# Kernel tuning notes

Measured on AMD Instinct MI355X. Metric: run time of the kernel, lower is better.

The kernel has to match this reference:

```python
import jax, jax.numpy as jnp
import numpy as np

N, DIM, K = 8192, 64, 32
ALPHA = 1.0

def setup_inputs() -> dict:
    key = jax.random.key(0)
    k1, k2, k3, k4, k5, k6 = jax.random.split(key, 6)
    s = 1.0 / np.sqrt(DIM)
    return {
        "node_emb": jax.random.normal(k1, (N, DIM), dtype=jnp.float32),
        "noise": jax.random.uniform(k2, (N, N), dtype=jnp.float32),
        "W1": jax.random.uniform(k3, (DIM, DIM), minval=-s, maxval=s, dtype=jnp.float32),
        "b1": jax.random.uniform(k4, (DIM,), minval=-s, maxval=s, dtype=jnp.float32),
        "W2": jax.random.uniform(k5, (DIM, DIM), minval=-s, maxval=s, dtype=jnp.float32),
        "b2": jax.random.uniform(k6, (DIM,), minval=-s, maxval=s, dtype=jnp.float32),
    }

def reference(node_emb, noise, W1, b1, W2, b2):
    # dual Linear + exact (erf) GELU, matching torch F.gelu default
    v1 = jax.nn.gelu(ALPHA * (node_emb @ W1.T + b1), approximate=False)  # [N, dim]
    v2 = jax.nn.gelu(ALPHA * (node_emb @ W2.T + b2), approximate=False)  # [N, dim]
    # asymmetric adjacency: relu(v1 v2^T - v2 v1^T)  -> [N, N]
    adj = jax.nn.relu(v1 @ v2.T - v2 @ v1.T)
    # top-k per row on noise-perturbed scores (tie-break), scatter 1s into mask
    _, idx = jax.lax.top_k(adj + noise * 0.01, K)            # idx: [N, K]
    mask = jnp.zeros((N, N), dtype=adj.dtype).at[jnp.arange(N)[:, None], idx].set(1.0)
    return adj * mask
```

## Files before the change

### kernel.cpp

```cpp
#include <hip/hip_runtime.h>
#include <math.h>


__global__ __launch_bounds__(256) void compute_vv(
    const float* __restrict__ emb, const float* __restrict__ W1,
    const float* __restrict__ b1, const float* __restrict__ W2,
    const float* __restrict__ b2, float* __restrict__ VV)
{
    __shared__ float sW[2][64 * 65];
    __shared__ float sb[2][64];
    __shared__ float semb[2][64];
    int tid = threadIdx.x;
    for (int t = tid; t < 64 * 64; t += 256) {
        int o = t >> 6, k = t & 63;
        sW[0][o * 65 + k] = W1[t];
        sW[1][o * 65 + k] = W2[t];
    }
    if (tid < 64) { sb[0][tid] = b1[tid]; sb[1][tid] = b2[tid]; }
    int i0 = blockIdx.x * 2;
    if (tid < 128) semb[tid >> 6][tid & 63] = emb[(size_t)i0 * 64 + tid];
    __syncthreads();

    int li = tid >> 7;
    int c  = tid & 127;
    int o  = c >> 1;
    int w  = c & 1;
    const float* wr = &sW[w][o * 65];
    const float* e  = &semb[li][0];
    float acc = 0.0f;
#pragma unroll
    for (int k = 0; k < 64; ++k) acc = fmaf(e[k], wr[k], acc);
    float x = acc + sb[w][o];
    double xd = (double)x;
    double g = 0.5 * xd * (1.0 + erf(xd * 0.70710678118654752440));
    VV[(size_t)(i0 + li) * 128 + c] = (float)g;
}

__global__ __launch_bounds__(256, 3) void adj_gemm_tri(
    const float* __restrict__ VV, float* __restrict__ out)
{
    int bi = blockIdx.x, bj = blockIdx.y;
    if (bj < bi) return;

    __shared__ __align__(16) float smem[8448];
    float* Ar1 = smem;
    float* Ar2 = smem + 2112;
    float* Ac1 = smem + 4224;
    float* Ac2 = smem + 6336;

    int tid  = threadIdx.x;
    int trow = tid >> 4, tcol = tid & 15;
    const int grow = bi * 128, gcol = bj * 128;

    float d1[8][8], d2[8][8];
#pragma unroll
    for (int r = 0; r < 8; ++r)
#pragma unroll
        for (int c = 0; c < 8; ++c) { d1[r][c] = 0.0f; d2[r][c] = 0.0f; }

    const float4* VV4 = (const float4*)VV;
    for (int kb = 0; kb < 4; ++kb) {
        __syncthreads();
#pragma unroll
        for (int g4 = 0; g4 < 4; ++g4) {
            int g = tid + g4 * 256;
            int row = g >> 3, off = g & 7;
            float4 f = VV4[(size_t)(grow + row) * 32 + kb * 8 + off];
            float4 h = VV4[(size_t)(gcol + row) * 32 + kb * 8 + off];
            int kk = off * 2;
            Ar1[kk * 132 + row] = f.x; Ar2[kk * 132 + row] = f.y;
            Ar1[(kk + 1) * 132 + row] = f.z; Ar2[(kk + 1) * 132 + row] = f.w;
            Ac1[kk * 132 + row] = h.x; Ac2[kk * 132 + row] = h.y;
            Ac1[(kk + 1) * 132 + row] = h.z; Ac2[(kk + 1) * 132 + row] = h.w;
        }
        __syncthreads();
#pragma unroll 2
        for (int k = 0; k < 16; ++k) {
            float rv1[8], rv2[8], cv1[8], cv2[8];
            *(float4*)&rv1[0] = *(const float4*)&Ar1[k * 132 + trow * 4];
            *(float4*)&rv1[4] = *(const float4*)&Ar1[k * 132 + 64 + trow * 4];
            *(float4*)&rv2[0] = *(const float4*)&Ar2[k * 132 + trow * 4];
            *(float4*)&rv2[4] = *(const float4*)&Ar2[k * 132 + 64 + trow * 4];
            *(float4*)&cv1[0] = *(const float4*)&Ac1[k * 132 + tcol * 4];
            *(float4*)&cv1[4] = *(const float4*)&Ac1[k * 132 + 64 + tcol * 4];
            *(float4*)&cv2[0] = *(const float4*)&Ac2[k * 132 + tcol * 4];
            *(float4*)&cv2[4] = *(const float4*)&Ac2[k * 132 + 64 + tcol * 4];
#pragma unroll
            for (int r = 0; r < 8; ++r)
#pragma unroll
                for (int c = 0; c < 8; ++c) {
                    d1[r][c] = fmaf(rv1[r], cv2[c], d1[r][c]);
                    d2[r][c] = fmaf(rv2[r], cv1[c], d2[r][c]);
                }
        }
    }

#pragma unroll
    for (int rr = 0; rr < 8; ++rr) {
        int r = (rr < 4) ? (trow * 4 + rr) : (64 + trow * 4 + (rr - 4));
        float4 o0, o1;
        o0.x = fmaxf(d1[rr][0] - d2[rr][0], 0.0f);
        o0.y = fmaxf(d1[rr][1] - d2[rr][1], 0.0f);
        o0.z = fmaxf(d1[rr][2] - d2[rr][2], 0.0f);
        o0.w = fmaxf(d1[rr][3] - d2[rr][3], 0.0f);
        o1.x = fmaxf(d1[rr][4] - d2[rr][4], 0.0f);
        o1.y = fmaxf(d1[rr][5] - d2[rr][5], 0.0f);
        o1.z = fmaxf(d1[rr][6] - d2[rr][6], 0.0f);
        o1.w = fmaxf(d1[rr][7] - d2[rr][7], 0.0f);
        float* op = out + (size_t)(grow + r) * 8192 + gcol;
        *(float4*)(op + tcol * 4)      = o0;
        *(float4*)(op + 64 + tcol * 4) = o1;
    }

    float (*tT)[132] = (float(*)[132])smem;
#pragma unroll
    for (int p = 0; p < 2; ++p) {
        __syncthreads();
#pragma unroll
        for (int cc4 = 0; cc4 < 4; ++cc4) {
            int cc = p * 4 + cc4;
            int cl = tcol * 4 + cc4;
            float4 lo, hi;
            lo.x = fmaxf(d2[0][cc] - d1[0][cc], 0.0f);
            lo.y = fmaxf(d2[1][cc] - d1[1][cc], 0.0f);
            lo.z = fmaxf(d2[2][cc] - d1[2][cc], 0.0f);
            lo.w = fmaxf(d2[3][cc] - d1[3][cc], 0.0f);
            hi.x = fmaxf(d2[4][cc] - d1[4][cc], 0.0f);
            hi.y = fmaxf(d2[5][cc] - d1[5][cc], 0.0f);
            hi.z = fmaxf(d2[6][cc] - d1[6][cc], 0.0f);
            hi.w = fmaxf(d2[7][cc] - d1[7][cc], 0.0f);
            *(float4*)&tT[cl][trow * 4]      = lo;
            *(float4*)&tT[cl][64 + trow * 4] = hi;
        }
        __syncthreads();
        for (int g = tid; g < 2048; g += 256) {
            int orow_ = g >> 5, off = g & 31;
            float4 v = *(const float4*)&tT[orow_][off * 4];
            *(float4*)(out + (size_t)(gcol + p * 64 + orow_) * 8192 + grow + off * 4) = v;
        }
    }
}

#define SKIPV 0.015625f
#define CAP   1024

__device__ __forceinline__ int binof(float s, float lo, float scale, float inv) {
    int b = (int)((s - lo) * scale);
    if (b > 1023) b = 1023;
    if (lo + (float)b * inv > s) --b;
    else if (b < 1023 && lo + (float)(b + 1) * inv <= s) ++b;
    return b;
}

__device__ __forceinline__ void select_bin1024(
    const unsigned* __restrict__ hist, unsigned* __restrict__ chs,
    int tid, int krem, int* __restrict__ sh_bin, int* __restrict__ sh_above,
    unsigned* __restrict__ sh_total)
{
    chs[tid] = hist[tid * 4 + 0] + hist[tid * 4 + 1] +
               hist[tid * 4 + 2] + hist[tid * 4 + 3];
    __syncthreads();
    if (tid < 64) {
        unsigned g = chs[tid * 4 + 0] + chs[tid * 4 + 1] +
                     chs[tid * 4 + 2] + chs[tid * 4 + 3];
        unsigned v = g;
#pragma unroll
        for (int off = 1; off < 64; off <<= 1) {
            unsigned o = __shfl_down(v, off);
            if (tid + off < 64) v += o;
        }
        if (tid == 0) *sh_total = v;
        unsigned above = v - g;
        if (above < (unsigned)krem && (unsigned)krem <= above + g) {
            unsigned cum = above;
            int bin = -1;
            for (int c = 3; c >= 0 && bin < 0; --c) {
                unsigned cs = chs[tid * 4 + c];
                if (cum + cs >= (unsigned)krem) {
                    int cb = tid * 4 + c;
                    for (int b = 3; b >= 0; --b) {
                        unsigned h = hist[cb * 4 + b];
                        if (cum + h >= (unsigned)krem) { bin = cb * 4 + b; break; }
                        cum += h;
                    }
                } else cum += cs;
            }
            *sh_bin = bin; *sh_above = (int)cum;
        }
    }
    __syncthreads();
}

__global__ __launch_bounds__(256, 4) void topk_linear(
    const float* __restrict__ noise, float* __restrict__ out)
{
    __shared__ unsigned hist[1024];
    __shared__ unsigned chs[256];
    __shared__ float    cs[CAP];
    __shared__ int      ci[CAP];
    __shared__ unsigned flags[256];
    __shared__ int      sh_bin, sh_above;
    __shared__ unsigned sh_total, sh_cnt;

    int tid = threadIdx.x;
    int row = blockIdx.x;
    float*       orow = out   + (size_t)row * 8192;
    const float* nrow = noise + (size_t)row * 8192;
    const float4* o4 = (const float4*)orow;
    const float4* n4 = (const float4*)nrow;

    float4 nv[8], av[8];
#pragma unroll
    for (int i = 0; i < 8; ++i) nv[i] = n4[tid + i * 256];
#pragma unroll
    for (int i = 0; i < 8; ++i) av[i] = o4[tid + i * 256];

    for (int i = tid; i < 1024; i += 256) hist[i] = 0u;
    flags[tid] = 0u;

    float ss[32];
#pragma unroll
    for (int i = 0; i < 8; ++i) {
        ss[i * 4 + 0] = __fadd_rn(av[i].x, __fmul_rn(nv[i].x, 0.01f));
        ss[i * 4 + 1] = __fadd_rn(av[i].y, __fmul_rn(nv[i].y, 0.01f));
        ss[i * 4 + 2] = __fadd_rn(av[i].z, __fmul_rn(nv[i].z, 0.01f));
        ss[i * 4 + 3] = __fadd_rn(av[i].w, __fmul_rn(nv[i].w, 0.01f));
    }
    __syncthreads();

#pragma unroll
    for (int s = 0; s < 32; ++s) {
        if (ss[s] >= SKIPV)
            atomicAdd(&hist[binof(ss[s], 0.0f, 128.0f, 0.0078125f)], 1u);
    }
    __syncthreads();

    select_bin1024(hist, chs, tid, 32, &sh_bin, &sh_above, &sh_total);
    float Tf, lo, width;
    int krem;
    if (sh_total >= 32u) {
        Tf    = (float)sh_bin * 0.0078125f;
        krem  = 32 - sh_above;
        lo    = Tf; width = 0.0078125f;
    } else {
        int kr2 = 32 - (int)sh_total;
        __syncthreads();
        for (int i = tid; i < 1024; i += 256) hist[i] = 0u;
        __syncthreads();
#pragma unroll
        for (int s = 0; s < 32; ++s) {
            if (ss[s] < SKIPV)
                atomicAdd(&hist[binof(ss[s], 0.0f, 65536.0f, 1.525878906e-5f)], 1u);
        }
        __syncthreads();
        select_bin1024(hist, chs, tid, kr2, &sh_bin, &sh_above, &sh_total);
        Tf    = (float)sh_bin * 1.525878906e-5f;
        krem  = kr2 - sh_above;
        lo    = Tf; width = 1.525878906e-5f;
    }

    int cnt;
    for (int pass = 0;; ++pass) {
        if (tid == 0) sh_cnt = 0u;
        __syncthreads();
#pragma unroll
        for (int s = 0; s < 32; ++s) {
            if (ss[s] >= Tf) {
                unsigned p = atomicAdd(&sh_cnt, 1u);
                if (p < CAP) {
                    cs[p] = ss[s];
                    ci[p] = tid * 4 + (s >> 2) * 1024 + (s & 3);
                }
            }
        }
        __syncthreads();
        cnt = (int)sh_cnt;
        if (cnt <= CAP || pass >= 2) break;
        for (int i = tid; i < 1024; i += 256) hist[i] = 0u;
        __syncthreads();
        float scale = 1024.0f / width;
        float inv   = width * 0.0009765625f;
#pragma unroll
        for (int s = 0; s < 32; ++s) {
            if (ss[s] >= lo && ss[s] < lo + width)
                atomicAdd(&hist[binof(ss[s], lo, scale, inv)], 1u);
        }
        __syncthreads();
        select_bin1024(hist, chs, tid, krem, &sh_bin, &sh_above, &sh_total);
        Tf    = lo + (float)sh_bin * inv;
        krem -= sh_above;
        lo    = Tf; width = inv;
    }
    if (cnt > CAP) cnt = CAP;

    float4 rv[8];
#pragma unroll
    for (int i = 0; i < 8; ++i) rv[i] = o4[tid + i * 256];

    for (int t = tid; t < cnt; t += 256) {
        float msv = cs[t];
        int   mi  = ci[t];
        int rank = 0;
        for (int j = 0; j < cnt; ++j) {
            float os = cs[j];
            rank += (os > msv || (os == msv && ci[j] < mi)) ? 1 : 0;
        }
        if (rank < 32) atomicOr(&flags[mi >> 5], 1u << (mi & 31));
    }
    __syncthreads();

#pragma unroll
    for (int i = 0; i < 8; ++i) {
        int j0 = 4 * (tid + i * 256);
        unsigned w = flags[j0 >> 5];
        int sh = j0 & 31;
        float4 o;
        o.x = ((w >> (sh + 0)) & 1u) ? rv[i].x : 0.0f;
        o.y = ((w >> (sh + 1)) & 1u) ? rv[i].y : 0.0f;
        o.z = ((w >> (sh + 2)) & 1u) ? rv[i].z : 0.0f;
        o.w = ((w >> (sh + 3)) & 1u) ? rv[i].w : 0.0f;
        ((float4*)orow)[tid + i * 256] = o;
    }
}

extern "C" void kernel_launch(void* const* d_in, const int* in_sizes, int n_in,
                              void* d_out, int out_size, void* d_ws, size_t ws_size,
                              hipStream_t stream) {
    (void)in_sizes; (void)n_in; (void)out_size; (void)ws_size;
    const float* emb   = (const float*)d_in[0];
    const float* noise = (const float*)d_in[1];
    const float* W1    = (const float*)d_in[2];
    const float* b1    = (const float*)d_in[3];
    const float* W2    = (const float*)d_in[4];
    const float* b2    = (const float*)d_in[5];
    float* out = (float*)d_out;
    float* VV  = (float*)d_ws;

    hipLaunchKernelGGL(compute_vv, dim3(4096), dim3(256), 0, stream,
                       emb, W1, b1, W2, b2, VV);
    hipLaunchKernelGGL(adj_gemm_tri, dim3(64, 64), dim3(256), 0, stream, VV, out);
    hipLaunchKernelGGL(topk_linear, dim3(8192), dim3(256), 0, stream, noise, out);
}
```

Measured before the change: 700.5 us.

## Load row operands directly from global memory, stage only column tile in LDS

The row-side A tile is no longer staged in shared memory. Each thread reads its 8 rows' float4 values straight from global memory inside the k-loop, and only the column-side tile goes through LDS, now in two larger k-blocks. This halves LDS staging and LDS reads and cuts the number of barriers. The cost is redundant global/L2 loads, since the 16 threads sharing a row reload the same data, plus higher register pressure, so launch bounds drop from 3 to 2 blocks per CU.

```diff
diff --git a/kernel.cpp b/kernel.cpp
--- a/kernel.cpp
+++ b/kernel.cpp
@@ -36,17 +36,15 @@
     VV[(size_t)(i0 + li) * 128 + c] = (float)g;
 }
 
-__global__ __launch_bounds__(256, 3) void adj_gemm_tri(
+__global__ __launch_bounds__(256, 2) void adj_gemm_tri(
     const float* __restrict__ VV, float* __restrict__ out)
 {
     int bi = blockIdx.x, bj = blockIdx.y;
     if (bj < bi) return;
 
     __shared__ __align__(16) float smem[8448];
-    float* Ar1 = smem;
-    float* Ar2 = smem + 2112;
-    float* Ac1 = smem + 4224;
-    float* Ac2 = smem + 6336;
+    float* Ac1 = smem;
+    float* Ac2 = smem + 4224;
 
     int tid  = threadIdx.x;
     int trow = tid >> 4, tcol = tid & 15;
@@ -59,39 +57,66 @@
         for (int c = 0; c < 8; ++c) { d1[r][c] = 0.0f; d2[r][c] = 0.0f; }
 
     const float4* VV4 = (const float4*)VV;
-    for (int kb = 0; kb < 4; ++kb) {
-        __syncthreads();
-#pragma unroll
-        for (int g4 = 0; g4 < 4; ++g4) {
-            int g = tid + g4 * 256;
-            int row = g >> 3, off = g & 7;
-            float4 f = VV4[(size_t)(grow + row) * 32 + kb * 8 + off];
-            float4 h = VV4[(size_t)(gcol + row) * 32 + kb * 8 + off];
+    const size_t rlo = (size_t)(grow + trow * 4) * 32;
+    const size_t rhi = (size_t)(grow + 64 + trow * 4) * 32;
+
+    for (int kb = 0; kb < 2; ++kb) {
+        __syncthreads();
+#pragma unroll
+        for (int it = 0; it < 8; ++it) {
+            int g = tid + it * 256;
+            int row = g >> 4, off = g & 15;
+            float4 h = VV4[(size_t)(gcol + row) * 32 + kb * 16 + off];
             int kk = off * 2;
-            Ar1[kk * 132 + row] = f.x; Ar2[kk * 132 + row] = f.y;
-            Ar1[(kk + 1) * 132 + row] = f.z; Ar2[(kk + 1) * 132 + row] = f.w;
             Ac1[kk * 132 + row] = h.x; Ac2[kk * 132 + row] = h.y;
             Ac1[(kk + 1) * 132 + row] = h.z; Ac2[(kk + 1) * 132 + row] = h.w;
         }
         __syncthreads();
+
 #pragma unroll 2
-        for (int k = 0; k < 16; ++k) {
-            float rv1[8], rv2[8], cv1[8], cv2[8];
-            *(float4*)&rv1[0] = *(const float4*)&Ar1[k * 132 + trow * 4];
-            *(float4*)&rv1[4] = *(const float4*)&Ar1[k * 132 + 64 + trow * 4];
-            *(float4*)&rv2[0] = *(const float4*)&Ar2[k * 132 + trow * 4];
-            *(float4*)&rv2[4] = *(const float4*)&Ar2[k * 132 + 64 + trow * 4];
-            *(float4*)&cv1[0] = *(const float4*)&Ac1[k * 132 + tcol * 4];
-            *(float4*)&cv1[4] = *(const float4*)&Ac1[k * 132 + 64 + tcol * 4];
-            *(float4*)&cv2[0] = *(const float4*)&Ac2[k * 132 + tcol * 4];
-            *(float4*)&cv2[4] = *(const float4*)&Ac2[k * 132 + 64 + tcol * 4];
-#pragma unroll
-            for (int r = 0; r < 8; ++r)
-#pragma unroll
-                for (int c = 0; c < 8; ++c) {
-                    d1[r][c] = fmaf(rv1[r], cv2[c], d1[r][c]);
-                    d2[r][c] = fmaf(rv2[r], cv1[c], d2[r][c]);
-                }
+        for (int ql = 0; ql < 16; ++ql) {
+            int q = kb * 16 + ql;
+            float4 f0 = VV4[rlo + 0 * 32 + q];
+            float4 f1 = VV4[rlo + 1 * 32 + q];
+            float4 f2 = VV4[rlo + 2 * 32 + q];
+            float4 f3 = VV4[rlo + 3 * 32 + q];
+            float4 f4 = VV4[rhi + 0 * 32 + q];
+            float4 f5 = VV4[rhi + 1 * 32 + q];
+            float4 f6 = VV4[rhi + 2 * 32 + q];
+            float4 f7 = VV4[rhi + 3 * 32 + q];
+
+            int k0 = ql * 2;
+            float cv1[8], cv2[8];
+            *(float4*)&cv1[0] = *(const float4*)&Ac1[k0 * 132 + tcol * 4];
+            *(float4*)&cv1[4] = *(const float4*)&Ac1[k0 * 132 + 64 + tcol * 4];
+            *(float4*)&cv2[0] = *(const float4*)&Ac2[k0 * 132 + tcol * 4];
+            *(float4*)&cv2[4] = *(const float4*)&Ac2[k0 * 132 + 64 + tcol * 4];
+            {
+                float rv1[8] = {f0.x, f1.x, f2.x, f3.x, f4.x, f5.x, f6.x, f7.x};
+                float rv2[8] = {f0.y, f1.y, f2.y, f3.y, f4.y, f5.y, f6.y, f7.y};
+#pragma unroll
+                for (int r = 0; r < 8; ++r)
+#pragma unroll
+                    for (int c = 0; c < 8; ++c) {
+                        d1[r][c] = fmaf(rv1[r], cv2[c], d1[r][c]);
+                        d2[r][c] = fmaf(rv2[r], cv1[c], d2[r][c]);
+                    }
+            }
+            *(float4*)&cv1[0] = *(const float4*)&Ac1[(k0 + 1) * 132 + tcol * 4];
+            *(float4*)&cv1[4] = *(const float4*)&Ac1[(k0 + 1) * 132 + 64 + tcol * 4];
+            *(float4*)&cv2[0] = *(const float4*)&Ac2[(k0 + 1) * 132 + tcol * 4];
+            *(float4*)&cv2[4] = *(const float4*)&Ac2[(k0 + 1) * 132 + 64 + tcol * 4];
+            {
+                float rv1[8] = {f0.z, f1.z, f2.z, f3.z, f4.z, f5.z, f6.z, f7.z};
+                float rv2[8] = {f0.w, f1.w, f2.w, f3.w, f4.w, f5.w, f6.w, f7.w};
+#pragma unroll
+                for (int r = 0; r < 8; ++r)
+#pragma unroll
+                    for (int c = 0; c < 8; ++c) {
+                        d1[r][c] = fmaf(rv1[r], cv2[c], d1[r][c]);
+                        d2[r][c] = fmaf(rv2[r], cv1[c], d2[r][c]);
+                    }
+            }
         }
     }
 
```

New measurement: 719.4 us. 2.7% more time.
